# Optimization experiments

Measured on AMD Instinct MI355X. Metric: run time of the kernel, lower is better.

Reference implementation:

```python
import jax, jax.numpy as jnp
import numpy as np

B, L, F = 16384, 64, 32
E, A, H = 64, 8, 128


def setup_inputs() -> dict:
    key = jax.random.key(0)
    ks = jax.random.split(key, 16)
    s = 0.1
    return {
        "lane_features": jax.random.normal(ks[0], (B, L, F), jnp.float32),
        "lane_mask": jax.random.randint(ks[1], (B, L), 0, 2).astype(jnp.float32),
        "action_mask": jax.random.randint(ks[2], (B, A), 0, 2).astype(jnp.float32),
        # SingleHeadAttentionPool params (stored [in,out])
        "W": jax.random.normal(ks[3], (F, F), jnp.float32) * s,
        "bW": jnp.zeros((F,), jnp.float32),
        "v": jax.random.normal(ks[4], (F,), jnp.float32) * s,
        "projW": jax.random.normal(ks[5], (F, E), jnp.float32) * s,
        "projb": jnp.zeros((E,), jnp.float32),
        # policy head MLP [E->128->128->A], tanh
        "piW1": jax.random.normal(ks[6], (E, H), jnp.float32) * s,
        "pib1": jnp.zeros((H,), jnp.float32),
        "piW2": jax.random.normal(ks[7], (H, H), jnp.float32) * s,
        "pib2": jnp.zeros((H,), jnp.float32),
        "piW3": jax.random.normal(ks[8], (H, A), jnp.float32) * s,
        "pib3": jnp.zeros((A,), jnp.float32),
        # value head MLP [E->128->128->1], tanh
        "vfW1": jax.random.normal(ks[9], (E, H), jnp.float32) * s,
        "vfb1": jnp.zeros((H,), jnp.float32),
        "vfW2": jax.random.normal(ks[10], (H, H), jnp.float32) * s,
        "vfb2": jnp.zeros((H,), jnp.float32),
        "vfW3": jax.random.normal(ks[11], (H, 1), jnp.float32) * s,
        "vfb3": jnp.zeros((1,), jnp.float32),
    }


def reference(lane_features, lane_mask, action_mask, W, bW, v, projW, projb,
              piW1, pib1, piW2, pib2, piW3, pib3,
              vfW1, vfb1, vfW2, vfb2, vfW3, vfb3):
    X = lane_features                       # [B,L,F]
    mask = lane_mask > 0.5                  # [B,L] bool
    has_active = jnp.any(mask, axis=-1)     # [B]

    # additive attention pool, masked softmax == gather-then-softmax
    Hh = jnp.tanh(jnp.einsum('blf,fg->blg', X, W) + bW)   # [B,L,F]
    scores = jnp.einsum('blf,f->bl', Hh, v)                # [B,L]
    NEG = jnp.float32(-1e30)
    w = jax.nn.softmax(jnp.where(mask, scores, NEG), axis=-1)
    w = jnp.where(mask, w, 0.0)
    pooled = jnp.einsum('bl,blf->bf', w, X)                # [B,F]
    z = pooled @ projW + projb                             # [B,E]
    z = jnp.where(has_active[:, None], z, 0.0)             # empty set -> zeros

    # heads
    h = jnp.tanh(z @ piW1 + pib1)
    h = jnp.tanh(h @ piW2 + pib2)
    logits = h @ piW3 + pib3                               # [B,A]

    g = jnp.tanh(z @ vfW1 + vfb1)
    g = jnp.tanh(g @ vfW2 + vfb2)
    value = (g @ vfW3 + vfb3)[:, 0]                        # [B]

    # hard action masking
    invalid = action_mask <= 0
    masked = jnp.where(invalid, jnp.finfo(logits.dtype).min, logits)
    all_invalid = jnp.all(invalid, axis=1)
    masked = jnp.where(all_invalid[:, None], logits, masked)
    return masked, value
```

## Files before the change

kernel.cpp:

```cpp
#include <hip/hip_runtime.h>
#include <float.h>

#define NBATCH 16384
#define SAFE_MAX 3.3e38f
#define SAFE_NEG -3.3e38f

typedef __attribute__((ext_vector_type(8))) short bf16x8;
typedef __attribute__((ext_vector_type(4))) float f32x4;

__device__ __forceinline__ float san(float v) {
    v = (v == v) ? v : 0.0f;
    return fminf(fmaxf(v, SAFE_NEG), SAFE_MAX);
}

__device__ __forceinline__ float tanh_fast(float a) {
    float e = __expf(a + a);
    return fmaf(-2.0f, __builtin_amdgcn_rcpf(e + 1.0f), 1.0f);
}

__device__ __forceinline__ unsigned short f2bf_rne(float v) {
    unsigned int u = __float_as_uint(v);
    return (unsigned short)((u + 0x7FFFu + ((u >> 16) & 1u)) >> 16);
}

extern "C" __global__ void __launch_bounds__(256, 4)
pool_v5(const float* __restrict__ X, const float* __restrict__ LM,
        const float* __restrict__ W, const float* __restrict__ bW,
        const float* __restrict__ vv,
        const float* __restrict__ projW, const float* __restrict__ projb,
        float* __restrict__ zout)
{
    __shared__ __align__(16) short wt[32 * 40];
    __shared__ float pool_s[4][32];

    const int tid  = threadIdx.x;
    const int w    = __builtin_amdgcn_readfirstlane(tid >> 6);
    const int lane = tid & 63;
    const int c    = lane & 15;
    const int quad = lane >> 4;
    const long b   = (long)blockIdx.x * 4 + w;

    for (int i = tid; i < 1024; i += 256) {
        const int n = i >> 5, k = i & 31;
        wt[n * 40 + k] = (short)f2bf_rne(W[k * 32 + n]);
    }

    float bwr[8], vvr[8];
#pragma unroll
    for (int u = 0; u < 2; ++u)
#pragma unroll
        for (int r = 0; r < 4; ++r) {
            const int g = 16 * u + 4 * quad + r;
            bwr[u * 4 + r] = bW[g];
            vvr[u * 4 + r] = vv[g];
        }
    const float pjb = projb[lane];

    float xr[4][8];
#pragma unroll
    for (int t = 0; t < 4; ++t) {
        const float4* p = (const float4*)(X + b * 2048 + (16 * t + c) * 32 + quad * 8);
        float4 a0 = p[0], a1 = p[1];
        xr[t][0] = a0.x; xr[t][1] = a0.y; xr[t][2] = a0.z; xr[t][3] = a0.w;
        xr[t][4] = a1.x; xr[t][5] = a1.y; xr[t][6] = a1.z; xr[t][7] = a1.w;
    }
    float ml[4];
#pragma unroll
    for (int t = 0; t < 4; ++t) ml[t] = LM[b * 64 + 16 * t + c];

    union { bf16x8 v; unsigned int u[4]; } afr[4];
#pragma unroll
    for (int t = 0; t < 4; ++t)
#pragma unroll
        for (int j2 = 0; j2 < 4; ++j2)
            afr[t].u[j2] = __builtin_amdgcn_perm(
                __float_as_uint(xr[t][2 * j2 + 1]),
                __float_as_uint(xr[t][2 * j2]), 0x07060302u);

    __syncthreads();

    union { bf16x8 v; uint4 q; } bfr[2];
#pragma unroll
    for (int u = 0; u < 2; ++u)
        bfr[u].q = *((const uint4*)&wt[(16 * u + c) * 40 + quad * 8]);

    float sp[4] = {0.f, 0.f, 0.f, 0.f};
#pragma unroll
    for (int u = 0; u < 2; ++u) {
        f32x4 a[4];
#pragma unroll
        for (int t = 0; t < 4; ++t) {
            a[t] = (f32x4){0.f, 0.f, 0.f, 0.f};
            a[t] = __builtin_amdgcn_mfma_f32_16x16x32_bf16(
                bfr[u].v, afr[t].v, a[t], 0, 0, 0);
        }
#pragma unroll
        for (int t = 0; t < 4; ++t)
#pragma unroll
            for (int r = 0; r < 4; ++r)
                sp[t] = fmaf(tanh_fast(a[t][r] + bwr[u * 4 + r]),
                             vvr[u * 4 + r], sp[t]);
    }

    float s[4];
#pragma unroll
    for (int t = 0; t < 4; ++t) {
        float v0 = sp[t];
        v0 += __shfl_xor(v0, 16);
        v0 += __shfl_xor(v0, 32);
        s[t] = v0;
    }

    bool act[4];
#pragma unroll
    for (int t = 0; t < 4; ++t) act[t] = ml[t] > 0.5f;

    float m = -1e30f;
#pragma unroll
    for (int t = 0; t < 4; ++t) m = fmaxf(m, act[t] ? s[t] : -1e30f);
    m = fmaxf(m, __shfl_xor(m, 1));
    m = fmaxf(m, __shfl_xor(m, 2));
    m = fmaxf(m, __shfl_xor(m, 4));
    m = fmaxf(m, __shfl_xor(m, 8));

    float ev[4];
    float es = 0.0f;
#pragma unroll
    for (int t = 0; t < 4; ++t) {
        ev[t] = act[t] ? __expf(s[t] - m) : 0.0f;
        es += ev[t];
    }
    es += __shfl_xor(es, 1);
    es += __shfl_xor(es, 2);
    es += __shfl_xor(es, 4);
    es += __shfl_xor(es, 8);
    const float rcpS = __builtin_amdgcn_rcpf(es);

    float wgt[4];
#pragma unroll
    for (int t = 0; t < 4; ++t)
        wgt[t] = (act[t] && es > 0.0f) ? ev[t] * rcpS : 0.0f;

#pragma unroll
    for (int j = 0; j < 8; ++j) {
        float p = wgt[0] * xr[0][j];
#pragma unroll
        for (int t = 1; t < 4; ++t) p = fmaf(wgt[t], xr[t][j], p);
        p += __shfl_xor(p, 1);
        p += __shfl_xor(p, 2);
        p += __shfl_xor(p, 4);
        p += __shfl_xor(p, 8);
        if (c == 0) pool_s[w][quad * 8 + j] = p;
    }
    asm volatile("s_waitcnt lgkmcnt(0)" ::: "memory");

    float zv = pjb;
#pragma unroll
    for (int f = 0; f < 32; ++f)
        zv = fmaf(pool_s[w][f], projW[f * 64 + lane], zv);
    const bool anyl = act[0] | act[1] | act[2] | act[3];
    const bool any = (__ballot(anyl) != 0ull);
    zout[b * 64 + lane] = any ? san(zv) : 0.0f;
}

#define ZT 0
#define H1 4160
#define PL 0
extern "C" __global__ void __launch_bounds__(512)
heads_kernel(const float* __restrict__ z, const float* __restrict__ AM,
             const float* __restrict__ piW1, const float* __restrict__ pib1,
             const float* __restrict__ piW2, const float* __restrict__ pib2,
             const float* __restrict__ piW3, const float* __restrict__ pib3,
             const float* __restrict__ vfW1, const float* __restrict__ vfb1,
             const float* __restrict__ vfW2, const float* __restrict__ vfb2,
             const float* __restrict__ vfW3, const float* __restrict__ vfb3,
             float* __restrict__ out)
{
    __shared__ float smem[12352];

    const int tid  = threadIdx.x;
    const int w    = __builtin_amdgcn_readfirstlane(tid >> 6);
    const int el   = tid & 63;
    const bool isPi = (blockIdx.x & 1) == 0;
    const int tile  = blockIdx.x >> 1;

    for (int i = tid; i < 4096; i += 512)
        smem[ZT + (i >> 6) * 65 + (i & 63)] = z[(long)tile * 4096 + i];
    __syncthreads();

    const float* W1 = isPi ? piW1 : vfW1;
    const float* b1 = isPi ? pib1 : vfb1;
    const float* W2 = isPi ? piW2 : vfW2;
    const float* b2 = isPi ? pib2 : vfb2;

    float acc[16];
#pragma unroll
    for (int i = 0; i < 16; ++i) acc[i] = b1[w * 16 + i];
#pragma unroll 8
    for (int e = 0; e < 64; ++e) {
        const float zv = smem[ZT + el * 65 + e];
        const float* wr = W1 + e * 128 + w * 16;
#pragma unroll
        for (int i = 0; i < 16; ++i) acc[i] = fmaf(zv, wr[i], acc[i]);
    }
#pragma unroll
    for (int i = 0; i < 16; ++i)
        smem[H1 + (w * 16 + i) * 64 + el] = tanh_fast(acc[i]);
    __syncthreads();

    float a2[16];
#pragma unroll
    for (int i = 0; i < 16; ++i) a2[i] = b2[w * 16 + i];
#pragma unroll 8
    for (int j = 0; j < 128; ++j) {
        const float hv = smem[H1 + j * 64 + el];
        const float* wr = W2 + j * 128 + w * 16;
#pragma unroll
        for (int i = 0; i < 16; ++i) a2[i] = fmaf(hv, wr[i], a2[i]);
    }

    if (isPi) {
        float pl[8];
#pragma unroll
        for (int a = 0; a < 8; ++a) pl[a] = 0.0f;
#pragma unroll
        for (int i = 0; i < 16; ++i) {
            const float h2 = tanh_fast(a2[i]);
            const float* wr = piW3 + (w * 16 + i) * 8;
#pragma unroll
            for (int a = 0; a < 8; ++a) pl[a] = fmaf(h2, wr[a], pl[a]);
        }
#pragma unroll
        for (int a = 0; a < 8; ++a)
            smem[PL + w * 512 + el * 8 + a] = pl[a];
        __syncthreads();

        const int rel = tid >> 3, ra = tid & 7;
        float lg = pib3[ra];
#pragma unroll
        for (int w2 = 0; w2 < 8; ++w2)
            lg += smem[PL + w2 * 512 + rel * 8 + ra];
        lg = san(lg);
        const long rb = (long)tile * 64 + rel;
        const float am = AM[rb * 8 + ra];
        const bool inv = (am <= 0.0f);
        const unsigned long long bal = __ballot(inv);
        const int grp = (tid & 63) >> 3;
        const bool allinv = (((bal >> (grp * 8)) & 0xFFull) == 0xFFull);
        out[rb * 8 + ra] = allinv ? lg : (inv ? SAFE_NEG : lg);
    } else {
        float pv = 0.0f;
#pragma unroll
        for (int i = 0; i < 16; ++i)
            pv = fmaf(tanh_fast(a2[i]), vfW3[w * 16 + i], pv);
        smem[PL + el * 8 + w] = pv;
        __syncthreads();

        if (tid < 64) {
            float val = vfb3[0];
#pragma unroll
            for (int w2 = 0; w2 < 8; ++w2) val += smem[PL + tid * 8 + w2];
            out[(long)NBATCH * 8 + (long)tile * 64 + tid] = san(val);
        }
    }
}

extern "C" __global__ void __launch_bounds__(512, 2)
fused_v4(const float* __restrict__ X, const float* __restrict__ LM,
         const float* __restrict__ AM,
         const float* __restrict__ W, const float* __restrict__ bW,
         const float* __restrict__ vv,
         const float* __restrict__ projW, const float* __restrict__ projb,
         const float* __restrict__ piW1, const float* __restrict__ pib1,
         const float* __restrict__ piW2, const float* __restrict__ pib2,
         const float* __restrict__ piW3, const float* __restrict__ pib3,
         const float* __restrict__ vfW1, const float* __restrict__ vfb1,
         const float* __restrict__ vfW2, const float* __restrict__ vfb2,
         const float* __restrict__ vfW3, const float* __restrict__ vfb3,
         float* __restrict__ out)
{
    __shared__ __align__(16) short wt[32 * 40];
    __shared__ float zl[64 * 33];
    __shared__ float pool_s[8][32];
    __shared__ float h1pi[128 * 32];
    __shared__ float h1v[128 * 32];
    __shared__ float plpi[8 * 256];
    __shared__ float plv[32 * 8];

    const int tid  = threadIdx.x;
    const int w    = __builtin_amdgcn_readfirstlane(tid >> 6);
    const int lane = tid & 63;
    const int c    = lane & 15;
    const int quad = lane >> 4;
    const long btile = (long)blockIdx.x * 32;

    for (int i = tid; i < 1024; i += 512) {
        const int n = i >> 5, k = i & 31;
        wt[n * 40 + k] = (short)f2bf_rne(W[k * 32 + n]);
    }

    float bwr[8], vvr[8];
#pragma unroll
    for (int u = 0; u < 2; ++u)
#pragma unroll
        for (int r = 0; r < 4; ++r) {
            const int g = 16 * u + 4 * quad + r;
            bwr[u * 4 + r] = bW[g];
            vvr[u * 4 + r] = vv[g];
        }
    const float pjb = projb[lane];

    __syncthreads();

    union { bf16x8 v; uint4 q; } bfr[2];
#pragma unroll
    for (int u = 0; u < 2; ++u)
        bfr[u].q = *((const uint4*)&wt[(16 * u + c) * 40 + quad * 8]);

#pragma unroll 1
    for (int it = 0; it < 4; ++it) {
        const int brel = w * 4 + it;
        const long b = btile + brel;

        float xr[4][8];
#pragma unroll
        for (int t = 0; t < 4; ++t) {
            const float4* p = (const float4*)(X + b * 2048 + (16 * t + c) * 32 + quad * 8);
            float4 a0 = p[0], a1 = p[1];
            xr[t][0] = a0.x; xr[t][1] = a0.y; xr[t][2] = a0.z; xr[t][3] = a0.w;
            xr[t][4] = a1.x; xr[t][5] = a1.y; xr[t][6] = a1.z; xr[t][7] = a1.w;
        }
        float ml[4];
#pragma unroll
        for (int t = 0; t < 4; ++t) ml[t] = LM[b * 64 + 16 * t + c];

        union { bf16x8 v; unsigned int u[4]; } afr[4];
#pragma unroll
        for (int t = 0; t < 4; ++t)
#pragma unroll
            for (int j2 = 0; j2 < 4; ++j2)
                afr[t].u[j2] = __builtin_amdgcn_perm(
                    __float_as_uint(xr[t][2 * j2 + 1]),
                    __float_as_uint(xr[t][2 * j2]), 0x07060302u);

        float sp[4] = {0.f, 0.f, 0.f, 0.f};
#pragma unroll
        for (int u = 0; u < 2; ++u) {
            f32x4 a[4];
#pragma unroll
            for (int t = 0; t < 4; ++t) {
                a[t] = (f32x4){0.f, 0.f, 0.f, 0.f};
                a[t] = __builtin_amdgcn_mfma_f32_16x16x32_bf16(
                    bfr[u].v, afr[t].v, a[t], 0, 0, 0);
            }
#pragma unroll
            for (int t = 0; t < 4; ++t)
#pragma unroll
                for (int r = 0; r < 4; ++r)
                    sp[t] = fmaf(tanh_fast(a[t][r] + bwr[u * 4 + r]),
                                 vvr[u * 4 + r], sp[t]);
        }

        float s[4];
#pragma unroll
        for (int t = 0; t < 4; ++t) {
            float v0 = sp[t];
            v0 += __shfl_xor(v0, 16);
            v0 += __shfl_xor(v0, 32);
            s[t] = v0;
        }

        bool act[4];
#pragma unroll
        for (int t = 0; t < 4; ++t) act[t] = ml[t] > 0.5f;

        float m = -1e30f;
#pragma unroll
        for (int t = 0; t < 4; ++t) m = fmaxf(m, act[t] ? s[t] : -1e30f);
        m = fmaxf(m, __shfl_xor(m, 1));
        m = fmaxf(m, __shfl_xor(m, 2));
        m = fmaxf(m, __shfl_xor(m, 4));
        m = fmaxf(m, __shfl_xor(m, 8));

        float ev[4];
        float es = 0.0f;
#pragma unroll
        for (int t = 0; t < 4; ++t) {
            ev[t] = act[t] ? __expf(s[t] - m) : 0.0f;
            es += ev[t];
        }
        es += __shfl_xor(es, 1);
        es += __shfl_xor(es, 2);
        es += __shfl_xor(es, 4);
        es += __shfl_xor(es, 8);
        const float rcpS = __builtin_amdgcn_rcpf(es);

        float wgt[4];
#pragma unroll
        for (int t = 0; t < 4; ++t)
            wgt[t] = (act[t] && es > 0.0f) ? ev[t] * rcpS : 0.0f;

#pragma unroll
        for (int j = 0; j < 8; ++j) {
            float p = wgt[0] * xr[0][j];
#pragma unroll
            for (int t = 1; t < 4; ++t) p = fmaf(wgt[t], xr[t][j], p);
            p += __shfl_xor(p, 1);
            p += __shfl_xor(p, 2);
            p += __shfl_xor(p, 4);
            p += __shfl_xor(p, 8);
            if (c == 0) pool_s[w][quad * 8 + j] = p;
        }
        asm volatile("s_waitcnt lgkmcnt(0)" ::: "memory");

        float zv = pjb;
#pragma unroll
        for (int f = 0; f < 32; ++f)
            zv = fmaf(pool_s[w][f], projW[f * 64 + lane], zv);
        const bool anyl = act[0] | act[1] | act[2] | act[3];
        const bool any = (__ballot(anyl) != 0ull);
        zl[lane * 33 + brel] = any ? san(zv) : 0.0f;
    }
    __syncthreads();

    const int el = lane & 31;
    const int hh = lane >> 5;
    const int w4 = w - 4;

    if (w < 4) {
        const int rb0 = w * 32 + hh * 16;
        float acc[16];
#pragma unroll
        for (int i = 0; i < 16; ++i) acc[i] = pib1[rb0 + i];
#pragma unroll 8
        for (int e = 0; e < 64; ++e) {
            const float zv = zl[e * 33 + el];
            const float* wr = piW1 + e * 128 + rb0;
#pragma unroll
            for (int i = 0; i < 16; ++i) acc[i] = fmaf(zv, wr[i], acc[i]);
        }
#pragma unroll
        for (int i = 0; i < 16; ++i)
            h1pi[(rb0 + i) * 32 + el] = tanh_fast(acc[i]);
    } else {
        const int rb0 = w4 * 32 + hh * 16;
        float acc[16];
#pragma unroll
        for (int i = 0; i < 16; ++i) acc[i] = vfb1[rb0 + i];
#pragma unroll 8
        for (int e = 0; e < 64; ++e) {
            const float zv = zl[e * 33 + el];
            const float* wr = vfW1 + e * 128 + rb0;
#pragma unroll
            for (int i = 0; i < 16; ++i) acc[i] = fmaf(zv, wr[i], acc[i]);
        }
#pragma unroll
        for (int i = 0; i < 16; ++i)
            h1v[(rb0 + i) * 32 + el] = tanh_fast(acc[i]);
    }
    __syncthreads();

    if (w < 4) {
        const int rb0 = w * 32 + hh * 16;
        const int g   = w * 2 + hh;
        float a2[16];
#pragma unroll
        for (int i = 0; i < 16; ++i) a2[i] = pib2[rb0 + i];
#pragma unroll 8
        for (int j = 0; j < 128; ++j) {
            const float hv = h1pi[j * 32 + el];
            const float* wr = piW2 + j * 128 + rb0;
#pragma unroll
            for (int i = 0; i < 16; ++i) a2[i] = fmaf(hv, wr[i], a2[i]);
        }
        float pl[8];
#pragma unroll
        for (int a = 0; a < 8; ++a) pl[a] = 0.0f;
#pragma unroll
        for (int i = 0; i < 16; ++i) {
            const float h2 = tanh_fast(a2[i]);
            const float* wr = piW3 + (rb0 + i) * 8;
#pragma unroll
            for (int a = 0; a < 8; ++a) pl[a] = fmaf(h2, wr[a], pl[a]);
        }
#pragma unroll
        for (int a = 0; a < 8; ++a)
            plpi[g * 256 + el * 8 + a] = pl[a];
    } else {
        const int rb0 = w4 * 32 + hh * 16;
        const int g   = w4 * 2 + hh;
        float a2[16];
#pragma unroll
        for (int i = 0; i < 16; ++i) a2[i] = vfb2[rb0 + i];
#pragma unroll 8
        for (int j = 0; j < 128; ++j) {
            const float hv = h1v[j * 32 + el];
            const float* wr = vfW2 + j * 128 + rb0;
#pragma unroll
            for (int i = 0; i < 16; ++i) a2[i] = fmaf(hv, wr[i], a2[i]);
        }
        float pv = 0.0f;
#pragma unroll
        for (int i = 0; i < 16; ++i)
            pv = fmaf(tanh_fast(a2[i]), vfW3[rb0 + i], pv);
        plv[el * 8 + g] = pv;
    }
    __syncthreads();

    if (w < 4) {
        const int rel = tid >> 3, ra = tid & 7;
        float lg = pib3[ra];
#pragma unroll
        for (int g2 = 0; g2 < 8; ++g2)
            lg += plpi[g2 * 256 + rel * 8 + ra];
        lg = san(lg);
        const long rb = btile + rel;
        const float am = AM[rb * 8 + ra];
        const bool inv = (am <= 0.0f);
        const unsigned long long bal = __ballot(inv);
        const int grp = (tid & 63) >> 3;
        const bool allinv = (((bal >> (grp * 8)) & 0xFFull) == 0xFFull);
        out[rb * 8 + ra] = allinv ? lg : (inv ? SAFE_NEG : lg);
    } else if (w == 4) {
        if (lane < 32) {
            float val = vfb3[0];
#pragma unroll
            for (int g2 = 0; g2 < 8; ++g2) val += plv[lane * 8 + g2];
            out[(long)NBATCH * 8 + btile + lane] = san(val);
        }
    }
}

extern "C" void kernel_launch(void* const* d_in, const int* in_sizes, int n_in,
                              void* d_out, int out_size, void* d_ws, size_t ws_size,
                              hipStream_t stream) {
    const float* X     = (const float*)d_in[0];
    const float* LM    = (const float*)d_in[1];
    const float* AM    = (const float*)d_in[2];
    const float* W     = (const float*)d_in[3];
    const float* bW    = (const float*)d_in[4];
    const float* vv    = (const float*)d_in[5];
    const float* projW = (const float*)d_in[6];
    const float* projb = (const float*)d_in[7];
    const float* piW1  = (const float*)d_in[8];
    const float* pib1  = (const float*)d_in[9];
    const float* piW2  = (const float*)d_in[10];
    const float* pib2  = (const float*)d_in[11];
    const float* piW3  = (const float*)d_in[12];
    const float* pib3  = (const float*)d_in[13];
    const float* vfW1  = (const float*)d_in[14];
    const float* vfb1  = (const float*)d_in[15];
    const float* vfW2  = (const float*)d_in[16];
    const float* vfb2  = (const float*)d_in[17];
    const float* vfW3  = (const float*)d_in[18];
    const float* vfb3  = (const float*)d_in[19];

    float* outp = (float*)d_out;
    const size_t zbytes = (size_t)NBATCH * 64 * sizeof(float);

    if (ws_size >= zbytes) {
        float* z = (float*)d_ws;
        pool_v5<<<NBATCH / 4, 256, 0, stream>>>(
            X, LM, W, bW, vv, projW, projb, z);
        heads_kernel<<<(NBATCH / 64) * 2, 512, 0, stream>>>(
            z, AM, piW1, pib1, piW2, pib2, piW3, pib3,
            vfW1, vfb1, vfW2, vfb2, vfW3, vfb3, outp);
    } else {
        fused_v4<<<NBATCH / 32, 512, 0, stream>>>(
            X, LM, AM, W, bW, vv, projW, projb,
            piW1, pib1, piW2, pib2, piW3, pib3,
            vfW1, vfb1, vfW2, vfb2, vfW3, vfb3, outp);
    }
}
```

Baseline: 257.0 us.

## Process two batch rows per wave with register prefetch of next row

Each wave in the pool kernel now handles two batch rows, loading the second row's lane features and mask into registers before computing the first. The grid is halved, which amortizes the per-block bf16 weight staging into LDS and hides global load latency behind compute. The cost is roughly doubled register use for X, which under launch_bounds(256,4) may cause spills or lower occupancy.

```diff
diff --git a/kernel.cpp b/kernel.cpp
--- a/kernel.cpp
+++ b/kernel.cpp
@@ -24,7 +24,7 @@
 }
 
 extern "C" __global__ void __launch_bounds__(256, 4)
-pool_v5(const float* __restrict__ X, const float* __restrict__ LM,
+pool_v7(const float* __restrict__ X, const float* __restrict__ LM,
         const float* __restrict__ W, const float* __restrict__ bW,
         const float* __restrict__ vv,
         const float* __restrict__ projW, const float* __restrict__ projb,
@@ -38,7 +38,7 @@
     const int lane = tid & 63;
     const int c    = lane & 15;
     const int quad = lane >> 4;
-    const long b   = (long)blockIdx.x * 4 + w;
+    const long b0  = ((long)blockIdx.x * 4 + w) * 2;
 
     for (int i = tid; i < 1024; i += 256) {
         const int n = i >> 5, k = i & 31;
@@ -59,23 +59,14 @@
     float xr[4][8];
 #pragma unroll
     for (int t = 0; t < 4; ++t) {
-        const float4* p = (const float4*)(X + b * 2048 + (16 * t + c) * 32 + quad * 8);
+        const float4* p = (const float4*)(X + b0 * 2048 + (16 * t + c) * 32 + quad * 8);
         float4 a0 = p[0], a1 = p[1];
         xr[t][0] = a0.x; xr[t][1] = a0.y; xr[t][2] = a0.z; xr[t][3] = a0.w;
         xr[t][4] = a1.x; xr[t][5] = a1.y; xr[t][6] = a1.z; xr[t][7] = a1.w;
     }
     float ml[4];
 #pragma unroll
-    for (int t = 0; t < 4; ++t) ml[t] = LM[b * 64 + 16 * t + c];
-
-    union { bf16x8 v; unsigned int u[4]; } afr[4];
-#pragma unroll
-    for (int t = 0; t < 4; ++t)
-#pragma unroll
-        for (int j2 = 0; j2 < 4; ++j2)
-            afr[t].u[j2] = __builtin_amdgcn_perm(
-                __float_as_uint(xr[t][2 * j2 + 1]),
-                __float_as_uint(xr[t][2 * j2]), 0x07060302u);
+    for (int t = 0; t < 4; ++t) ml[t] = LM[b0 * 64 + 16 * t + c];
 
     __syncthreads();
 
@@ -84,83 +75,121 @@
     for (int u = 0; u < 2; ++u)
         bfr[u].q = *((const uint4*)&wt[(16 * u + c) * 40 + quad * 8]);
 
-    float sp[4] = {0.f, 0.f, 0.f, 0.f};
-#pragma unroll
-    for (int u = 0; u < 2; ++u) {
-        f32x4 a[4];
+#pragma unroll 1
+    for (int it = 0; it < 2; ++it) {
+        const long b = b0 + it;
+
+        float xn[4][8];
+        float mn[4];
+        if (it == 0) {
+            const long bn = b0 + 1;
+#pragma unroll
+            for (int t = 0; t < 4; ++t) {
+                const float4* p = (const float4*)(X + bn * 2048 + (16 * t + c) * 32 + quad * 8);
+                float4 a0 = p[0], a1 = p[1];
+                xn[t][0] = a0.x; xn[t][1] = a0.y; xn[t][2] = a0.z; xn[t][3] = a0.w;
+                xn[t][4] = a1.x; xn[t][5] = a1.y; xn[t][6] = a1.z; xn[t][7] = a1.w;
+            }
+#pragma unroll
+            for (int t = 0; t < 4; ++t) mn[t] = LM[bn * 64 + 16 * t + c];
+        }
+
+        union { bf16x8 v; unsigned int u[4]; } afr[4];
+#pragma unroll
+        for (int t = 0; t < 4; ++t)
+#pragma unroll
+            for (int j2 = 0; j2 < 4; ++j2)
+                afr[t].u[j2] = __builtin_amdgcn_perm(
+                    __float_as_uint(xr[t][2 * j2 + 1]),
+                    __float_as_uint(xr[t][2 * j2]), 0x07060302u);
+
+        float sp[4] = {0.f, 0.f, 0.f, 0.f};
+#pragma unroll
+        for (int u = 0; u < 2; ++u) {
+            f32x4 a[4];
+#pragma unroll
+            for (int t = 0; t < 4; ++t) {
+                a[t] = (f32x4){0.f, 0.f, 0.f, 0.f};
+                a[t] = __builtin_amdgcn_mfma_f32_16x16x32_bf16(
+                    bfr[u].v, afr[t].v, a[t], 0, 0, 0);
+            }
+#pragma unroll
+            for (int t = 0; t < 4; ++t)
+#pragma unroll
+                for (int r = 0; r < 4; ++r)
+                    sp[t] = fmaf(tanh_fast(a[t][r] + bwr[u * 4 + r]),
+                                 vvr[u * 4 + r], sp[t]);
+        }
+
+        float s[4];
 #pragma unroll
         for (int t = 0; t < 4; ++t) {
-            a[t] = (f32x4){0.f, 0.f, 0.f, 0.f};
-            a[t] = __builtin_amdgcn_mfma_f32_16x16x32_bf16(
-                bfr[u].v, afr[t].v, a[t], 0, 0, 0);
-        }
+            float v0 = sp[t];
+            v0 += __shfl_xor(v0, 16);
+            v0 += __shfl_xor(v0, 32);
+            s[t] = v0;
+        }
+
+        bool act[4];
+#pragma unroll
+        for (int t = 0; t < 4; ++t) act[t] = ml[t] > 0.5f;
+
+        float m = -1e30f;
+#pragma unroll
+        for (int t = 0; t < 4; ++t) m = fmaxf(m, act[t] ? s[t] : -1e30f);
+        m = fmaxf(m, __shfl_xor(m, 1));
+        m = fmaxf(m, __shfl_xor(m, 2));
+        m = fmaxf(m, __shfl_xor(m, 4));
+        m = fmaxf(m, __shfl_xor(m, 8));
+
+        float ev[4];
+        float es = 0.0f;
+#pragma unroll
+        for (int t = 0; t < 4; ++t) {
+            ev[t] = act[t] ? __expf(s[t] - m) : 0.0f;
+            es += ev[t];
+        }
+        es += __shfl_xor(es, 1);
+        es += __shfl_xor(es, 2);
+        es += __shfl_xor(es, 4);
+        es += __shfl_xor(es, 8);
+        const float rcpS = __builtin_amdgcn_rcpf(es);
+
+        float wgt[4];
 #pragma unroll
         for (int t = 0; t < 4; ++t)
-#pragma unroll
-            for (int r = 0; r < 4; ++r)
-                sp[t] = fmaf(tanh_fast(a[t][r] + bwr[u * 4 + r]),
-                             vvr[u * 4 + r], sp[t]);
-    }
-
-    float s[4];
-#pragma unroll
-    for (int t = 0; t < 4; ++t) {
-        float v0 = sp[t];
-        v0 += __shfl_xor(v0, 16);
-        v0 += __shfl_xor(v0, 32);
-        s[t] = v0;
-    }
-
-    bool act[4];
-#pragma unroll
-    for (int t = 0; t < 4; ++t) act[t] = ml[t] > 0.5f;
-
-    float m = -1e30f;
-#pragma unroll
-    for (int t = 0; t < 4; ++t) m = fmaxf(m, act[t] ? s[t] : -1e30f);
-    m = fmaxf(m, __shfl_xor(m, 1));
-    m = fmaxf(m, __shfl_xor(m, 2));
-    m = fmaxf(m, __shfl_xor(m, 4));
-    m = fmaxf(m, __shfl_xor(m, 8));
-
-    float ev[4];
-    float es = 0.0f;
-#pragma unroll
-    for (int t = 0; t < 4; ++t) {
-        ev[t] = act[t] ? __expf(s[t] - m) : 0.0f;
-        es += ev[t];
-    }
-    es += __shfl_xor(es, 1);
-    es += __shfl_xor(es, 2);
-    es += __shfl_xor(es, 4);
-    es += __shfl_xor(es, 8);
-    const float rcpS = __builtin_amdgcn_rcpf(es);
-
-    float wgt[4];
-#pragma unroll
-    for (int t = 0; t < 4; ++t)
-        wgt[t] = (act[t] && es > 0.0f) ? ev[t] * rcpS : 0.0f;
-
-#pragma unroll
-    for (int j = 0; j < 8; ++j) {
-        float p = wgt[0] * xr[0][j];
-#pragma unroll
-        for (int t = 1; t < 4; ++t) p = fmaf(wgt[t], xr[t][j], p);
-        p += __shfl_xor(p, 1);
-        p += __shfl_xor(p, 2);
-        p += __shfl_xor(p, 4);
-        p += __shfl_xor(p, 8);
-        if (c == 0) pool_s[w][quad * 8 + j] = p;
-    }
-    asm volatile("s_waitcnt lgkmcnt(0)" ::: "memory");
-
-    float zv = pjb;
-#pragma unroll
-    for (int f = 0; f < 32; ++f)
-        zv = fmaf(pool_s[w][f], projW[f * 64 + lane], zv);
-    const bool anyl = act[0] | act[1] | act[2] | act[3];
-    const bool any = (__ballot(anyl) != 0ull);
-    zout[b * 64 + lane] = any ? san(zv) : 0.0f;
+            wgt[t] = (act[t] && es > 0.0f) ? ev[t] * rcpS : 0.0f;
+
+#pragma unroll
+        for (int j = 0; j < 8; ++j) {
+            float p = wgt[0] * xr[0][j];
+#pragma unroll
+            for (int t = 1; t < 4; ++t) p = fmaf(wgt[t], xr[t][j], p);
+            p += __shfl_xor(p, 1);
+            p += __shfl_xor(p, 2);
+            p += __shfl_xor(p, 4);
+            p += __shfl_xor(p, 8);
+            if (c == 0) pool_s[w][quad * 8 + j] = p;
+        }
+        asm volatile("s_waitcnt lgkmcnt(0)" ::: "memory");
+
+        float zv = pjb;
+#pragma unroll
+        for (int f = 0; f < 32; ++f)
+            zv = fmaf(pool_s[w][f], projW[f * 64 + lane], zv);
+        const bool anyl = act[0] | act[1] | act[2] | act[3];
+        const bool any = (__ballot(anyl) != 0ull);
+        zout[b * 64 + lane] = any ? san(zv) : 0.0f;
+
+        if (it == 0) {
+#pragma unroll
+            for (int t = 0; t < 4; ++t) {
+#pragma unroll
+                for (int j = 0; j < 8; ++j) xr[t][j] = xn[t][j];
+                ml[t] = mn[t];
+            }
+        }
+    }
 }
 
 #define ZT 0
@@ -560,7 +589,7 @@
 
     if (ws_size >= zbytes) {
         float* z = (float*)d_ws;
-        pool_v5<<<NBATCH / 4, 256, 0, stream>>>(
+        pool_v7<<<NBATCH / 8, 256, 0, stream>>>(
             X, LM, W, bW, vv, projW, projb, z);
         heads_kernel<<<(NBATCH / 64) * 2, 512, 0, stream>>>(
             z, AM, piW1, pib1, piW2, pib2, piW3, pib3,
```

Result: slower. 330.0 us (+28.4%).

## Process four rows per wave with async global-to-LDS prefetch of next row

Applied to the files above, without the earlier changes.

The pool kernel now has each wave handle four consecutive batch rows in a loop instead of one. While the current row is computed from registers, the next row's lane features are prefetched into a per-wave LDS buffer with global_load_lds and an XOR swizzle, and the next mask values go into registers. The grid shrinks by a factor of four. The aim is to hide global-load latency and amortise the per-block setup (weight conversion, bias loads), at the cost of 32KB of LDS per block and fewer resident waves in flight.

```diff
diff --git a/kernel.cpp b/kernel.cpp
--- a/kernel.cpp
+++ b/kernel.cpp
@@ -23,14 +23,31 @@
     return (unsigned short)((u + 0x7FFFu + ((u >> 16) & 1u)) >> 16);
 }
 
+#if defined(__has_builtin)
+#if __has_builtin(__builtin_amdgcn_global_load_lds)
+#define HAVE_GLL 1
+#endif
+#endif
+
+__device__ __forceinline__ void gload_lds16(const void* g, void* l, int lane) {
+#ifdef HAVE_GLL
+    __builtin_amdgcn_global_load_lds(
+        (const __attribute__((address_space(1))) void*)g,
+        (__attribute__((address_space(3))) void*)l, 16, 0, 0);
+#else
+    *(uint4*)((char*)l + lane * 16) = *(const uint4*)((const char*)g + 0);
+#endif
+}
+
 extern "C" __global__ void __launch_bounds__(256, 4)
-pool_v5(const float* __restrict__ X, const float* __restrict__ LM,
+pool_v9(const float* __restrict__ X, const float* __restrict__ LM,
         const float* __restrict__ W, const float* __restrict__ bW,
         const float* __restrict__ vv,
         const float* __restrict__ projW, const float* __restrict__ projb,
         float* __restrict__ zout)
 {
     __shared__ __align__(16) short wt[32 * 40];
+    __shared__ __align__(16) float xb[4][2048];
     __shared__ float pool_s[4][32];
 
     const int tid  = threadIdx.x;
@@ -38,7 +55,7 @@
     const int lane = tid & 63;
     const int c    = lane & 15;
     const int quad = lane >> 4;
-    const long b   = (long)blockIdx.x * 4 + w;
+    const long e0  = ((long)blockIdx.x * 4 + w) * 4;
 
     for (int i = tid; i < 1024; i += 256) {
         const int n = i >> 5, k = i & 31;
@@ -56,26 +73,27 @@
         }
     const float pjb = projb[lane];
 
+    const int gsw = (lane * 16) ^ (((lane >> 3) & 7) << 4);
+    {
+        const char* gsrc = (const char*)X + (e0 + 1) * 8192 + gsw;
+#pragma unroll
+        for (int j = 0; j < 8; ++j)
+            gload_lds16(gsrc + j * 1024, (char*)xb[w] + j * 1024, lane);
+    }
+
     float xr[4][8];
 #pragma unroll
     for (int t = 0; t < 4; ++t) {
-        const float4* p = (const float4*)(X + b * 2048 + (16 * t + c) * 32 + quad * 8);
+        const float4* p = (const float4*)(X + e0 * 2048 + (16 * t + c) * 32 + quad * 8);
         float4 a0 = p[0], a1 = p[1];
         xr[t][0] = a0.x; xr[t][1] = a0.y; xr[t][2] = a0.z; xr[t][3] = a0.w;
         xr[t][4] = a1.x; xr[t][5] = a1.y; xr[t][6] = a1.z; xr[t][7] = a1.w;
     }
-    float ml[4];
-#pragma unroll
-    for (int t = 0; t < 4; ++t) ml[t] = LM[b * 64 + 16 * t + c];
-
-    union { bf16x8 v; unsigned int u[4]; } afr[4];
-#pragma unroll
-    for (int t = 0; t < 4; ++t)
-#pragma unroll
-        for (int j2 = 0; j2 < 4; ++j2)
-            afr[t].u[j2] = __builtin_amdgcn_perm(
-                __float_as_uint(xr[t][2 * j2 + 1]),
-                __float_as_uint(xr[t][2 * j2]), 0x07060302u);
+    float ml[4], mln[4];
+#pragma unroll
+    for (int t = 0; t < 4; ++t) ml[t]  = LM[e0 * 64 + 16 * t + c];
+#pragma unroll
+    for (int t = 0; t < 4; ++t) mln[t] = LM[(e0 + 1) * 64 + 16 * t + c];
 
     __syncthreads();
 
@@ -84,83 +102,124 @@
     for (int u = 0; u < 2; ++u)
         bfr[u].q = *((const uint4*)&wt[(16 * u + c) * 40 + quad * 8]);
 
-    float sp[4] = {0.f, 0.f, 0.f, 0.f};
-#pragma unroll
-    for (int u = 0; u < 2; ++u) {
-        f32x4 a[4];
+    const int rsw = (c & 7) << 4;
+
+#pragma unroll 1
+    for (int k = 0; k < 4; ++k) {
+        const long b = e0 + k;
+
+        union { bf16x8 v; unsigned int u[4]; } afr[4];
+#pragma unroll
+        for (int t = 0; t < 4; ++t)
+#pragma unroll
+            for (int j2 = 0; j2 < 4; ++j2)
+                afr[t].u[j2] = __builtin_amdgcn_perm(
+                    __float_as_uint(xr[t][2 * j2 + 1]),
+                    __float_as_uint(xr[t][2 * j2]), 0x07060302u);
+
+        float sp[4] = {0.f, 0.f, 0.f, 0.f};
+#pragma unroll
+        for (int u = 0; u < 2; ++u) {
+            f32x4 a[4];
+#pragma unroll
+            for (int t = 0; t < 4; ++t) {
+                a[t] = (f32x4){0.f, 0.f, 0.f, 0.f};
+                a[t] = __builtin_amdgcn_mfma_f32_16x16x32_bf16(
+                    bfr[u].v, afr[t].v, a[t], 0, 0, 0);
+            }
+#pragma unroll
+            for (int t = 0; t < 4; ++t)
+#pragma unroll
+                for (int r = 0; r < 4; ++r)
+                    sp[t] = fmaf(tanh_fast(a[t][r] + bwr[u * 4 + r]),
+                                 vvr[u * 4 + r], sp[t]);
+        }
+
+        float s[4];
 #pragma unroll
         for (int t = 0; t < 4; ++t) {
-            a[t] = (f32x4){0.f, 0.f, 0.f, 0.f};
-            a[t] = __builtin_amdgcn_mfma_f32_16x16x32_bf16(
-                bfr[u].v, afr[t].v, a[t], 0, 0, 0);
-        }
+            float v0 = sp[t];
+            v0 += __shfl_xor(v0, 16);
+            v0 += __shfl_xor(v0, 32);
+            s[t] = v0;
+        }
+
+        bool act[4];
+#pragma unroll
+        for (int t = 0; t < 4; ++t) act[t] = ml[t] > 0.5f;
+
+        float m = -1e30f;
+#pragma unroll
+        for (int t = 0; t < 4; ++t) m = fmaxf(m, act[t] ? s[t] : -1e30f);
+        m = fmaxf(m, __shfl_xor(m, 1));
+        m = fmaxf(m, __shfl_xor(m, 2));
+        m = fmaxf(m, __shfl_xor(m, 4));
+        m = fmaxf(m, __shfl_xor(m, 8));
+
+        float ev[4];
+        float es = 0.0f;
+#pragma unroll
+        for (int t = 0; t < 4; ++t) {
+            ev[t] = act[t] ? __expf(s[t] - m) : 0.0f;
+            es += ev[t];
+        }
+        es += __shfl_xor(es, 1);
+        es += __shfl_xor(es, 2);
+        es += __shfl_xor(es, 4);
+        es += __shfl_xor(es, 8);
+        const float rcpS = __builtin_amdgcn_rcpf(es);
+
+        float wgt[4];
 #pragma unroll
         for (int t = 0; t < 4; ++t)
-#pragma unroll
-            for (int r = 0; r < 4; ++r)
-                sp[t] = fmaf(tanh_fast(a[t][r] + bwr[u * 4 + r]),
-                             vvr[u * 4 + r], sp[t]);
-    }
-
-    float s[4];
-#pragma unroll
-    for (int t = 0; t < 4; ++t) {
-        float v0 = sp[t];
-        v0 += __shfl_xor(v0, 16);
-        v0 += __shfl_xor(v0, 32);
-        s[t] = v0;
-    }
-
-    bool act[4];
-#pragma unroll
-    for (int t = 0; t < 4; ++t) act[t] = ml[t] > 0.5f;
-
-    float m = -1e30f;
-#pragma unroll
-    for (int t = 0; t < 4; ++t) m = fmaxf(m, act[t] ? s[t] : -1e30f);
-    m = fmaxf(m, __shfl_xor(m, 1));
-    m = fmaxf(m, __shfl_xor(m, 2));
-    m = fmaxf(m, __shfl_xor(m, 4));
-    m = fmaxf(m, __shfl_xor(m, 8));
-
-    float ev[4];
-    float es = 0.0f;
-#pragma unroll
-    for (int t = 0; t < 4; ++t) {
-        ev[t] = act[t] ? __expf(s[t] - m) : 0.0f;
-        es += ev[t];
-    }
-    es += __shfl_xor(es, 1);
-    es += __shfl_xor(es, 2);
-    es += __shfl_xor(es, 4);
-    es += __shfl_xor(es, 8);
-    const float rcpS = __builtin_amdgcn_rcpf(es);
-
-    float wgt[4];
-#pragma unroll
-    for (int t = 0; t < 4; ++t)
-        wgt[t] = (act[t] && es > 0.0f) ? ev[t] * rcpS : 0.0f;
-
-#pragma unroll
-    for (int j = 0; j < 8; ++j) {
-        float p = wgt[0] * xr[0][j];
-#pragma unroll
-        for (int t = 1; t < 4; ++t) p = fmaf(wgt[t], xr[t][j], p);
-        p += __shfl_xor(p, 1);
-        p += __shfl_xor(p, 2);
-        p += __shfl_xor(p, 4);
-        p += __shfl_xor(p, 8);
-        if (c == 0) pool_s[w][quad * 8 + j] = p;
-    }
-    asm volatile("s_waitcnt lgkmcnt(0)" ::: "memory");
-
-    float zv = pjb;
-#pragma unroll
-    for (int f = 0; f < 32; ++f)
-        zv = fmaf(pool_s[w][f], projW[f * 64 + lane], zv);
-    const bool anyl = act[0] | act[1] | act[2] | act[3];
-    const bool any = (__ballot(anyl) != 0ull);
-    zout[b * 64 + lane] = any ? san(zv) : 0.0f;
+            wgt[t] = (act[t] && es > 0.0f) ? ev[t] * rcpS : 0.0f;
+
+#pragma unroll
+        for (int j = 0; j < 8; ++j) {
+            float p = wgt[0] * xr[0][j];
+#pragma unroll
+            for (int t = 1; t < 4; ++t) p = fmaf(wgt[t], xr[t][j], p);
+            p += __shfl_xor(p, 1);
+            p += __shfl_xor(p, 2);
+            p += __shfl_xor(p, 4);
+            p += __shfl_xor(p, 8);
+            if (c == 0) pool_s[w][quad * 8 + j] = p;
+        }
+        asm volatile("s_waitcnt lgkmcnt(0)" ::: "memory");
+
+        float zv = pjb;
+#pragma unroll
+        for (int f = 0; f < 32; ++f)
+            zv = fmaf(pool_s[w][f], projW[f * 64 + lane], zv);
+        const bool anyl = act[0] | act[1] | act[2] | act[3];
+        const bool any = (__ballot(anyl) != 0ull);
+        zout[b * 64 + lane] = any ? san(zv) : 0.0f;
+
+        if (k == 3) break;
+
+        asm volatile("s_waitcnt vmcnt(1)" ::: "memory");
+#pragma unroll
+        for (int t = 0; t < 4; ++t) {
+            const int a0 = (((16 * t + c) * 128 + quad * 32) ^ rsw);
+            const uint4 v0 = *(const uint4*)((const char*)xb[w] + a0);
+            const uint4 v1 = *(const uint4*)((const char*)xb[w] + (a0 ^ 16));
+            xr[t][0] = __uint_as_float(v0.x); xr[t][1] = __uint_as_float(v0.y);
+            xr[t][2] = __uint_as_float(v0.z); xr[t][3] = __uint_as_float(v0.w);
+            xr[t][4] = __uint_as_float(v1.x); xr[t][5] = __uint_as_float(v1.y);
+            xr[t][6] = __uint_as_float(v1.z); xr[t][7] = __uint_as_float(v1.w);
+        }
+        asm volatile("s_waitcnt lgkmcnt(0)" ::: "memory");
+#pragma unroll
+        for (int t = 0; t < 4; ++t) ml[t] = mln[t];
+        if (k < 2) {
+            const char* gsrc = (const char*)X + (b + 2) * 8192 + gsw;
+#pragma unroll
+            for (int j = 0; j < 8; ++j)
+                gload_lds16(gsrc + j * 1024, (char*)xb[w] + j * 1024, lane);
+#pragma unroll
+            for (int t = 0; t < 4; ++t) mln[t] = LM[(b + 2) * 64 + 16 * t + c];
+        }
+    }
 }
 
 #define ZT 0
@@ -560,7 +619,7 @@
 
     if (ws_size >= zbytes) {
         float* z = (float*)d_ws;
-        pool_v5<<<NBATCH / 4, 256, 0, stream>>>(
+        pool_v9<<<NBATCH / 16, 256, 0, stream>>>(
             X, LM, W, bW, vv, projW, projb, z);
         heads_kernel<<<(NBATCH / 64) * 2, 512, 0, stream>>>(
             z, AM, piW1, pib1, piW2, pib2, piW3, pib3,
```

Result: slower. 299.4 us (+16.5%).
